# Kernel optimization log

Hardware: AMD Instinct MI355X
Metric: run time of the kernel (lower is better)

## Reference

```python
import jax, jax.numpy as jnp
import numpy as np

N_NODES = 50000      # nodes
N_EDGES = 800000     # edges (avg degree 16)
D = 128              # input_dim == hidden_dim
C = 32               # output_dim (classes)
G = 64               # number of graphs in batch
EPS = 1e-5           # LayerNorm eps (torch default)
NUM_LAYERS = 3


def setup_inputs() -> dict:
    key = jax.random.key(0)
    ks = jax.random.split(key, 12)
    scale = 1.0 / np.sqrt(D)
    x = jax.random.normal(ks[0], (N_NODES, D), dtype=jnp.float32)
    edge_index = jax.random.randint(ks[1], (2, N_EDGES), 0, N_NODES)
    batch = jnp.sort(jax.random.randint(ks[2], (N_NODES,), 0, G))
    # CustomConv params: self-loop linear + message linear, 3 layers stacked
    W_self = jax.random.normal(ks[3], (NUM_LAYERS, D, D), dtype=jnp.float32) * scale
    b_self = jnp.zeros((NUM_LAYERS, D), dtype=jnp.float32)
    W_msg = jax.random.normal(ks[4], (NUM_LAYERS, D, D), dtype=jnp.float32) * scale
    b_msg = jnp.zeros((NUM_LAYERS, D), dtype=jnp.float32)
    # two LayerNorms (after layers 0 and 1)
    ln_g = jnp.ones((2, D), dtype=jnp.float32)
    ln_b = jnp.zeros((2, D), dtype=jnp.float32)
    # post-MP MLP head: Linear(D,D) -> Dropout(identity in eval) -> Linear(D,C)
    W1 = jax.random.normal(ks[5], (D, D), dtype=jnp.float32) * scale
    b1 = jnp.zeros((D,), dtype=jnp.float32)
    W2 = jax.random.normal(ks[6], (D, C), dtype=jnp.float32) * scale
    b2 = jnp.zeros((C,), dtype=jnp.float32)
    return {"x": x, "W_self": W_self, "b_self": b_self, "W_msg": W_msg,
            "b_msg": b_msg, "ln_g": ln_g, "ln_b": ln_b, "W1": W1, "b1": b1,
            "W2": W2, "b2": b2, "edge_index": edge_index, "batch": batch}


def _layer_norm(h, g, b):
    mu = jnp.mean(h, axis=-1, keepdims=True)
    var = jnp.mean(jnp.square(h - mu), axis=-1, keepdims=True)
    return g * (h - mu) * jax.lax.rsqrt(var + EPS) + b


def reference(x, W_self, b_self, W_msg, b_msg, ln_g, ln_b, W1, b1, W2, b2,
              edge_index, batch):
    src, dst = edge_index[0], edge_index[1]
    for i in range(NUM_LAYERS):
        # CustomConv: self linear + sum-aggregated neighbor messages
        msg = x @ W_msg[i] + b_msg[i]                     # [N, D]
        agg = jax.ops.segment_sum(msg[src], dst, num_segments=N_NODES)
        x = x @ W_self[i] + b_self[i] + agg               # [N, D]
        x = jax.nn.relu(x)
        # dropout p=0.25 is identity in eval mode
        if i != NUM_LAYERS - 1:
            x = _layer_norm(x, ln_g[i], ln_b[i])
    # global mean pool over graphs
    sums = jax.ops.segment_sum(x, batch, num_segments=G)          # [G, D]
    cnt = jax.ops.segment_sum(jnp.ones((N_NODES,), x.dtype), batch,
                              num_segments=G)                     # [G]
    pooled = sums / jnp.maximum(cnt, 1.0)[:, None]
    # post-MP head (dropout identity in eval)
    h = pooled @ W1 + b1
    logits = h @ W2 + b2                                          # [G, C]
    return jax.nn.log_softmax(logits, axis=1)
```

## Files before the change

### kernel.cpp

```cpp
#include <hip/hip_runtime.h>
#include <hip/hip_bf16.h>
#include <math.h>

#define N_NODES 50000
#define N_EDGES 800000
#define DIM 128
#define CLS 32
#define NGRAPH 64
#define LN_EPS 1e-5f
#define NBLK 196
#define ABLK 256
#define EPB (N_EDGES / ABLK)
#define EB_STRIDE 7168
#define LCAP 8192
#define ROWS1 (N_NODES + 1)

typedef __attribute__((ext_vector_type(8))) short bf16x8;
typedef __attribute__((ext_vector_type(4))) float f32x4;

static __device__ __forceinline__ int lower_bound_i(const int* a, int n, int key) {
    int lo = 0, hi = n;
    while (lo < hi) { int mid = (lo + hi) >> 1; if (a[mid] < key) lo = mid + 1; else hi = mid; }
    return lo;
}


__global__ __launch_bounds__(256) void prep_kernel(
    const float* __restrict__ x, const float* __restrict__ Wself,
    const float* __restrict__ Wmsg, __hip_bfloat16* __restrict__ XbIn,
    __hip_bfloat16* __restrict__ WT,
    int* __restrict__ ecur, float* __restrict__ gsum,
    __hip_bfloat16* __restrict__ padA, __hip_bfloat16* __restrict__ padB,
    __hip_bfloat16* __restrict__ padC, __hip_bfloat16* __restrict__ padD) {
    int i = blockIdx.x * 256 + threadIdx.x;
    if (i < N_NODES * DIM / 2) {
        float2 v = ((const float2*)x)[i];
        ((__hip_bfloat162*)XbIn)[i] = __float22bfloat162_rn(v);
    }
    if (i < 3 * 128 * 256) {
        int l = i / (128 * 256);
        int rem = i - l * (128 * 256);
        int n = rem >> 8;
        int k = rem & 255;
        float v = (k < 128) ? Wself[l * 16384 + k * 128 + n]
                            : Wmsg[l * 16384 + (k - 128) * 128 + n];
        WT[i] = __float2bfloat16(v);
    }
    if (i < NBLK) ecur[i] = i * EB_STRIDE;
    if (i < NGRAPH * DIM) gsum[i] = 0.f;
    if (i < DIM) {
        padA[i] = __float2bfloat16(0.f);
        padB[i] = __float2bfloat16(0.f);
        padC[i] = __float2bfloat16(0.f);
        padD[i] = __float2bfloat16(0.f);
    }
}


__global__ __launch_bounds__(1024) void bucket_kernel(
    const int* __restrict__ esrc, const int* __restrict__ edst,
    int* __restrict__ ecur, int* __restrict__ ebuf) {
    __shared__ int bc4[4][NBLK];
    __shared__ int bc[NBLK], bres[NBLK], bcnt[NBLK];
    const int t = threadIdx.x;
    const int e0 = blockIdx.x * EPB;
    for (int i = t; i < 4 * NBLK; i += 1024) ((int*)bc4)[i] = 0;
    __syncthreads();
    int dr[4], sr[4];
#pragma unroll
    for (int it = 0; it < 4; it++) {
        int i = t + it * 1024;
        if (i < EPB) { dr[it] = edst[e0 + i]; sr[it] = esrc[e0 + i]; }
        else { dr[it] = -1; sr[it] = 0; }
    }
    const int cpy = (t >> 6) & 3;
#pragma unroll
    for (int it = 0; it < 4; it++)
        if (dr[it] >= 0) atomicAdd(&bc4[cpy][dr[it] >> 8], 1);
    __syncthreads();
    if (t < NBLK) {
        int c = bc4[0][t] + bc4[1][t] + bc4[2][t] + bc4[3][t];
        int r = (c + 7) & ~7;
        int res = atomicAdd(&ecur[t], r);
        bres[t] = res;
        bcnt[t] = c;
        bc[t] = res;
    }
    __syncthreads();
#pragma unroll
    for (int it = 0; it < 4; it++)
        if (dr[it] >= 0) {
            int d = dr[it];
            int pos = atomicAdd(&bc[d >> 8], 1);
            ebuf[pos] = ((d & 255) << 16) | sr[it];
        }
    __syncthreads();
    if (t < NBLK) {
        int c = bcnt[t], r = (c + 7) & ~7, base = bres[t];
        for (int j = c; j < r; j++) ebuf[base + j] = -1;
    }
}


__global__ __launch_bounds__(1024) void csr_fused_kernel(
    const int* __restrict__ ebuf, const int* __restrict__ ecur,
    int* __restrict__ counts, int* __restrict__ off, int* __restrict__ csr) {
    __shared__ int ncnt[256];
    __shared__ int ssc[256];
    __shared__ int cur[256];
    __shared__ int lcsr[LCAP];
    const int b = blockIdx.x, t = threadIdx.x;
    const int used = ecur[b] - b * EB_STRIDE;
    const int* eb = ebuf + b * EB_STRIDE;
    for (int i = t; i < LCAP; i += 1024) lcsr[i] = N_NODES;
    if (t < 256) ncnt[t] = 0;
    __syncthreads();
    for (int i = t; i < used; i += 1024) {
        int p = eb[i];
        if (p != -1) atomicAdd(&ncnt[p >> 16], 1);
    }
    __syncthreads();
    int myc = 0, mypad = 0;
    const int gi = b * 256 + t;
    if (t < 256) {
        myc = (gi < N_NODES) ? ncnt[t] : 0;
        mypad = (myc + 7) & ~7;
        ssc[t] = mypad;
    }
    __syncthreads();
    for (int o = 1; o < 256; o <<= 1) {
        int v = 0;
        if (t < 256 && t >= o) v = ssc[t - o];
        __syncthreads();
        if (t < 256) ssc[t] += v;
        __syncthreads();
    }
    if (t < 256) {
        int eoff = ssc[t] - mypad;
        cur[t] = eoff;
        if (gi < N_NODES) {
            off[gi] = b * LCAP + eoff;
            counts[gi] = myc;
        }
    }
    __syncthreads();
    for (int i = t; i < used; i += 1024) {
        int p = eb[i];
        if (p != -1) {
            int pos = atomicAdd(&cur[p >> 16], 1);
            lcsr[pos] = p & 0xFFFF;
        }
    }
    __syncthreads();
    const int total = ssc[255];
    int4* dst4 = (int4*)(csr + b * LCAP);
    const int4* src4 = (const int4*)lcsr;
    for (int i = t; i < (total >> 2); i += 1024) dst4[i] = src4[i];
}


__global__ __launch_bounds__(256) void agg_kernel(const __hip_bfloat16* __restrict__ Xb,
                                                  const int* __restrict__ off,
                                                  const int* __restrict__ counts,
                                                  const int* __restrict__ csr,
                                                  __hip_bfloat16* __restrict__ Sb) {
    const int wave = threadIdx.x >> 6;
    const int lane = threadIdx.x & 63;
    const int n = blockIdx.x * 4 + wave;
    if (n >= N_NODES) return;
    const int seg = lane >> 4;
    const int cl = lane & 15;
    int b = off[n];
    int e = b + ((counts[n] + 7) & ~7);
    float ac[8];
#pragma unroll
    for (int j = 0; j < 8; j++) ac[j] = 0.f;
    int base = b;
    for (; base + 16 <= e; base += 16) {
        int idx16 = csr[base + (lane & 15)];
        int s[4];
        uint4 v[4];
#pragma unroll
        for (int r = 0; r < 4; r++) s[r] = __shfl(idx16, r * 4 + seg, 64);
#pragma unroll
        for (int r = 0; r < 4; r++)
            v[r] = *(const uint4*)(Xb + (size_t)s[r] * DIM + cl * 8);
#pragma unroll
        for (int r = 0; r < 4; r++) {
            unsigned int u[4] = {v[r].x, v[r].y, v[r].z, v[r].w};
#pragma unroll
            for (int k = 0; k < 4; k++) {
                union { unsigned int b32; float f; } lo, hi;
                lo.b32 = u[k] << 16;
                hi.b32 = u[k] & 0xffff0000u;
                ac[2 * k] += lo.f;
                ac[2 * k + 1] += hi.f;
            }
        }
    }
    if (base < e) {
        int idx8 = csr[base + (lane & 7)];
        int s0 = __shfl(idx8, seg, 64);
        int s1 = __shfl(idx8, 4 + seg, 64);
        uint4 v0 = *(const uint4*)(Xb + (size_t)s0 * DIM + cl * 8);
        uint4 v1 = *(const uint4*)(Xb + (size_t)s1 * DIM + cl * 8);
        unsigned int u[8] = {v0.x, v0.y, v0.z, v0.w, v1.x, v1.y, v1.z, v1.w};
#pragma unroll
        for (int k = 0; k < 8; k++) {
            union { unsigned int b32; float f; } lo, hi;
            lo.b32 = u[k] << 16;
            hi.b32 = u[k] & 0xffff0000u;
            ac[2 * (k & 3)] += lo.f;
            ac[2 * (k & 3) + 1] += hi.f;
        }
    }
#pragma unroll
    for (int j = 0; j < 8; j++) {
        ac[j] += __shfl_xor(ac[j], 16, 64);
        ac[j] += __shfl_xor(ac[j], 32, 64);
    }
    if (lane < 16) {
        union { uint4 u; __hip_bfloat162 h[4]; } pk;
#pragma unroll
        for (int k = 0; k < 4; k++)
            pk.h[k] = __float22bfloat162_rn(make_float2(ac[2 * k], ac[2 * k + 1]));
        *(uint4*)(Sb + (size_t)n * DIM + cl * 8) = pk.u;
    }
}


__global__ __launch_bounds__(256) void layer_mfma_kernel(
    const __hip_bfloat16* __restrict__ Xb, const __hip_bfloat16* __restrict__ Sb,
    const __hip_bfloat16* __restrict__ WT,
    const float* __restrict__ bself, const float* __restrict__ bmsg,
    const int* __restrict__ deg,
    const float* __restrict__ lng, const float* __restrict__ lnb,
    const int* __restrict__ batch, float* __restrict__ gsum,
    __hip_bfloat16* __restrict__ XoutB, int do_ln, int do_pool) {
    __shared__ __hip_bfloat16 wlds[128 * 136];
    const int tid = threadIdx.x;
    const int w = tid >> 6, lane = tid & 63;
    const int l15 = lane & 15, q = lane >> 4;

    const int row = blockIdx.x * 64 + w * 16 + l15;
    const int rowc = min(row, N_NODES);

    f32x4 acc[8];
#pragma unroll
    for (int ct = 0; ct < 8; ct++) acc[ct] = (f32x4){0.f, 0.f, 0.f, 0.f};

    const __hip_bfloat16* Abase[2] = {Xb, Sb};
    for (int c = 0; c < 2; c++) {
        __syncthreads();
        {
            int n = tid >> 1, h = tid & 1;
            const uint4* src = (const uint4*)(WT + n * 256 + c * 128 + h * 64);
            uint4* dst = (uint4*)(&wlds[n * 136 + h * 64]);
#pragma unroll
            for (int i = 0; i < 8; i++) dst[i] = src[i];
        }
        __syncthreads();
        const __hip_bfloat16* arow = Abase[c] + (size_t)rowc * DIM;
#pragma unroll
        for (int ks = 0; ks < 4; ks++) {
            bf16x8 afrag = *(const bf16x8*)(arow + ks * 32 + q * 8);
#pragma unroll
            for (int ct = 0; ct < 8; ct++) {
                bf16x8 bfrag = *(const bf16x8*)(&wlds[(ct * 16 + l15) * 136 + ks * 32 + q * 8]);
                acc[ct] = __builtin_amdgcn_mfma_f32_16x16x32_bf16(afrag, bfrag, acc[ct], 0, 0, 0);
            }
        }
    }

    const int growbase = blockIdx.x * 64 + w * 16;
    float racc[8];
#pragma unroll
    for (int ct = 0; ct < 8; ct++) racc[ct] = 0.f;
    int gw = 0;
    bool fastp = false;
    if (do_pool) {
        int first = (growbase < N_NODES) ? growbase : (N_NODES - 1);
        gw = batch[first];
        int lastrow = growbase + 15;
        fastp = (growbase < N_NODES) && (lastrow < N_NODES) && (batch[lastrow] == gw);
    }
#pragma unroll
    for (int r = 0; r < 4; r++) {
        int grow = growbase + q * 4 + r;
        bool valid = grow < N_NODES;
        float dg = valid ? (float)deg[grow] : 0.f;
        float v[8];
        float s1 = 0.f;
#pragma unroll
        for (int ct = 0; ct < 8; ct++) {
            int col = ct * 16 + l15;
            float h = acc[ct][r] + bself[col] + dg * bmsg[col];
            h = fmaxf(h, 0.f);
            v[ct] = h;
            s1 += h;
        }
        if (do_ln) {
#pragma unroll
            for (int m = 1; m < 16; m <<= 1) s1 += __shfl_xor(s1, m, 64);
            float mu = s1 * (1.0f / 128.0f);
            float s2 = 0.f;
#pragma unroll
            for (int ct = 0; ct < 8; ct++) { float d = v[ct] - mu; s2 += d * d; }
#pragma unroll
            for (int m = 1; m < 16; m <<= 1) s2 += __shfl_xor(s2, m, 64);
            float rs = rsqrtf(s2 * (1.0f / 128.0f) + LN_EPS);
#pragma unroll
            for (int ct = 0; ct < 8; ct++) {
                int col = ct * 16 + l15;
                v[ct] = lng[col] * (v[ct] - mu) * rs + lnb[col];
            }
        }
        if (do_pool) {
            if (fastp) {
#pragma unroll
                for (int ct = 0; ct < 8; ct++) racc[ct] += v[ct];
            } else if (valid) {
                int g = batch[grow];
#pragma unroll
                for (int ct = 0; ct < 8; ct++)
                    atomicAdd(&gsum[g * DIM + ct * 16 + l15], v[ct]);
            }
        } else if (valid) {
#pragma unroll
            for (int ct = 0; ct < 8; ct++) {
                int col = ct * 16 + l15;
                XoutB[(size_t)grow * DIM + col] = __float2bfloat16(v[ct]);
            }
        }
    }
    if (do_pool && fastp) {
#pragma unroll
        for (int ct = 0; ct < 8; ct++) {
            racc[ct] += __shfl_xor(racc[ct], 16, 64);
            racc[ct] += __shfl_xor(racc[ct], 32, 64);
        }
        if (q == 0) {
#pragma unroll
            for (int ct = 0; ct < 8; ct++)
                atomicAdd(&gsum[gw * DIM + ct * 16 + l15], racc[ct]);
        }
    }
}


__global__ __launch_bounds__(128) void head_kernel(
    const float* __restrict__ gsum, const int* __restrict__ batch,
    const float* __restrict__ W1, const float* __restrict__ b1,
    const float* __restrict__ W2, const float* __restrict__ b2,
    float* __restrict__ out) {
    __shared__ float p[128];
    __shared__ float hh[128];
    int g = blockIdx.x;
    int j = threadIdx.x;
    int lo = lower_bound_i(batch, N_NODES, g);
    int hi = lower_bound_i(batch, N_NODES, g + 1);
    float cnt = fmaxf((float)(hi - lo), 1.0f);
    p[j] = gsum[g * DIM + j] / cnt;
    __syncthreads();
    float s = b1[j];
    for (int k = 0; k < DIM; k++) s += p[k] * W1[k * DIM + j];
    hh[j] = s;
    __syncthreads();
    if (j < CLS) {
        float l = b2[j];
        for (int k = 0; k < DIM; k++) l += hh[k] * W2[k * CLS + j];
        float mx = l;
#pragma unroll
        for (int m = 16; m >= 1; m >>= 1) mx = fmaxf(mx, __shfl_xor(mx, m, 64));
        float ex = expf(l - mx);
        float se = ex;
#pragma unroll
        for (int m = 16; m >= 1; m >>= 1) se += __shfl_xor(se, m, 64);
        out[g * CLS + j] = l - mx - logf(se);
    }
}


extern "C" void kernel_launch(void* const* d_in, const int* in_sizes, int n_in,
                              void* d_out, int out_size, void* d_ws, size_t ws_size,
                              hipStream_t stream) {
    (void)in_sizes; (void)n_in; (void)out_size; (void)ws_size;
    const float* x     = (const float*)d_in[0];
    const float* Wself = (const float*)d_in[1];
    const float* bself = (const float*)d_in[2];
    const float* Wmsg  = (const float*)d_in[3];
    const float* bmsg  = (const float*)d_in[4];
    const float* lng   = (const float*)d_in[5];
    const float* lnb   = (const float*)d_in[6];
    const float* W1    = (const float*)d_in[7];
    const float* b1    = (const float*)d_in[8];
    const float* W2    = (const float*)d_in[9];
    const float* b2    = (const float*)d_in[10];
    const int*   ei    = (const int*)d_in[11];
    const int*   batch = (const int*)d_in[12];
    const int* esrc = ei;
    const int* edst = ei + N_EDGES;

    char* w = (char*)d_ws;
    size_t o = 0;
    auto alloc = [&](size_t bytes) { void* p = w + o; o += (bytes + 255) & ~(size_t)255; return p; };
    __hip_bfloat16* XbIn = (__hip_bfloat16*)alloc((size_t)ROWS1 * DIM * 2);
    __hip_bfloat16* Xb0  = (__hip_bfloat16*)alloc((size_t)ROWS1 * DIM * 2);
    __hip_bfloat16* Xb1  = (__hip_bfloat16*)alloc((size_t)ROWS1 * DIM * 2);
    __hip_bfloat16* Sb   = (__hip_bfloat16*)alloc((size_t)ROWS1 * DIM * 2);
    __hip_bfloat16* WT   = (__hip_bfloat16*)alloc((size_t)3 * 128 * 256 * 2);
    int*   counts = (int*)alloc((size_t)N_NODES * 4);
    int*   offs   = (int*)alloc((size_t)(N_NODES + 1) * 4);
    int*   ecur   = (int*)alloc((size_t)NBLK * 4);
    int*   ebuf   = (int*)alloc((size_t)NBLK * EB_STRIDE * 4);
    int*   csr    = (int*)alloc((size_t)NBLK * LCAP * 4);
    float* gsum   = (float*)alloc((size_t)NGRAPH * DIM * 4);

    prep_kernel<<<(N_NODES * DIM / 2 + 255) / 256, 256, 0, stream>>>(
        x, Wself, Wmsg, XbIn, WT, ecur, gsum,
        XbIn + (size_t)N_NODES * DIM, Xb0 + (size_t)N_NODES * DIM,
        Xb1 + (size_t)N_NODES * DIM, Sb + (size_t)N_NODES * DIM);

    bucket_kernel<<<ABLK, 1024, 0, stream>>>(esrc, edst, ecur, ebuf);
    csr_fused_kernel<<<NBLK, 1024, 0, stream>>>(ebuf, ecur, counts, offs, csr);

    const __hip_bfloat16* XbCur = XbIn;
    __hip_bfloat16* bbufs[3] = {Xb0, Xb1, Xb0};
    for (int i = 0; i < 3; i++) {
        agg_kernel<<<(N_NODES + 3) / 4, 256, 0, stream>>>(XbCur, offs, counts, csr, Sb);
        layer_mfma_kernel<<<(N_NODES + 63) / 64, 256, 0, stream>>>(
            XbCur, Sb, WT + (size_t)i * 128 * 256,
            bself + i * DIM, bmsg + i * DIM, counts,
            (i < 2) ? lng + i * DIM : lng, (i < 2) ? lnb + i * DIM : lnb,
            batch, gsum,
            bbufs[i], (i < 2) ? 1 : 0, (i == 2) ? 1 : 0);
        XbCur = bbufs[i];
    }

    head_kernel<<<NGRAPH, 128, 0, stream>>>(gsum, batch, W1, b1, W2, b2, (float*)d_out);
}
```

Measured before the change: 263.1 us.

## Fuse neighbor aggregation into the MFMA layer kernel and shrink CSR to u16

Removes the separate aggregation kernel. Each wave of the layer kernel now gathers neighbor features for its 16 rows, two nodes at a time, and writes the sums into LDS, where the second MFMA pass reads them. This drops the global round trip of the aggregated buffer and three launches. The CSR source indices are stored as 16-bit values, halving index traffic. The cost is less gather parallelism per block, since 782 blocks now do the gathering where 12500 did before, plus extra LDS use that may lower occupancy.

```diff
diff --git a/kernel.cpp b/kernel.cpp
--- a/kernel.cpp
+++ b/kernel.cpp
@@ -24,6 +24,43 @@
     return lo;
 }
 
+static __device__ __forceinline__ void acc8(float* ac, uint4 v) {
+    unsigned int u[4] = {v.x, v.y, v.z, v.w};
+#pragma unroll
+    for (int k = 0; k < 4; k++) {
+        union { unsigned int b; float f; } lo, hi;
+        lo.b = u[k] << 16;
+        hi.b = u[k] & 0xffff0000u;
+        ac[2 * k] += lo.f;
+        ac[2 * k + 1] += hi.f;
+    }
+}
+
+static __device__ __forceinline__ void drain_node(const __hip_bfloat16* __restrict__ Xb,
+                                                  const unsigned short* __restrict__ csr,
+                                                  int b, int e, int seg, int cl, float* ac) {
+    for (; b + 16 <= e; b += 16) {
+        int idx16 = csr[b + cl];
+        int s[4];
+        uint4 v[4];
+#pragma unroll
+        for (int r = 0; r < 4; r++) s[r] = __shfl(idx16, r * 4 + seg, 64);
+#pragma unroll
+        for (int r = 0; r < 4; r++) v[r] = *(const uint4*)(Xb + (size_t)s[r] * DIM + cl * 8);
+#pragma unroll
+        for (int r = 0; r < 4; r++) acc8(ac, v[r]);
+    }
+    if (b < e) {
+        int idx8 = csr[b + (cl & 7)];
+        int s0 = __shfl(idx8, seg, 64);
+        int s1 = __shfl(idx8, 4 + seg, 64);
+        uint4 v0 = *(const uint4*)(Xb + (size_t)s0 * DIM + cl * 8);
+        uint4 v1 = *(const uint4*)(Xb + (size_t)s1 * DIM + cl * 8);
+        acc8(ac, v0);
+        acc8(ac, v1);
+    }
+}
+
 
 __global__ __launch_bounds__(256) void prep_kernel(
     const float* __restrict__ x, const float* __restrict__ Wself,
@@ -31,7 +68,7 @@
     __hip_bfloat16* __restrict__ WT,
     int* __restrict__ ecur, float* __restrict__ gsum,
     __hip_bfloat16* __restrict__ padA, __hip_bfloat16* __restrict__ padB,
-    __hip_bfloat16* __restrict__ padC, __hip_bfloat16* __restrict__ padD) {
+    __hip_bfloat16* __restrict__ padC) {
     int i = blockIdx.x * 256 + threadIdx.x;
     if (i < N_NODES * DIM / 2) {
         float2 v = ((const float2*)x)[i];
@@ -52,7 +89,6 @@
         padA[i] = __float2bfloat16(0.f);
         padB[i] = __float2bfloat16(0.f);
         padC[i] = __float2bfloat16(0.f);
-        padD[i] = __float2bfloat16(0.f);
     }
 }
 
@@ -104,15 +140,17 @@
 
 __global__ __launch_bounds__(1024) void csr_fused_kernel(
     const int* __restrict__ ebuf, const int* __restrict__ ecur,
-    int* __restrict__ counts, int* __restrict__ off, int* __restrict__ csr) {
+    int* __restrict__ counts, int* __restrict__ off,
+    unsigned short* __restrict__ csr) {
     __shared__ int ncnt[256];
     __shared__ int ssc[256];
     __shared__ int cur[256];
-    __shared__ int lcsr[LCAP];
+    __shared__ unsigned short lcsr[LCAP];
     const int b = blockIdx.x, t = threadIdx.x;
     const int used = ecur[b] - b * EB_STRIDE;
     const int* eb = ebuf + b * EB_STRIDE;
-    for (int i = t; i < LCAP; i += 1024) lcsr[i] = N_NODES;
+    for (int i = t; i < LCAP / 2; i += 1024)
+        ((unsigned int*)lcsr)[i] = 0xC350C350u;
     if (t < 256) ncnt[t] = 0;
     __syncthreads();
     for (int i = t; i < used; i += 1024) {
@@ -148,131 +186,131 @@
         int p = eb[i];
         if (p != -1) {
             int pos = atomicAdd(&cur[p >> 16], 1);
-            lcsr[pos] = p & 0xFFFF;
+            lcsr[pos] = (unsigned short)(p & 0xFFFF);
         }
     }
     __syncthreads();
     const int total = ssc[255];
-    int4* dst4 = (int4*)(csr + b * LCAP);
+    int4* dst4 = (int4*)(csr + (size_t)b * LCAP);
     const int4* src4 = (const int4*)lcsr;
-    for (int i = t; i < (total >> 2); i += 1024) dst4[i] = src4[i];
-}
-
-
-__global__ __launch_bounds__(256) void agg_kernel(const __hip_bfloat16* __restrict__ Xb,
-                                                  const int* __restrict__ off,
-                                                  const int* __restrict__ counts,
-                                                  const int* __restrict__ csr,
-                                                  __hip_bfloat16* __restrict__ Sb) {
-    const int wave = threadIdx.x >> 6;
-    const int lane = threadIdx.x & 63;
-    const int n = blockIdx.x * 4 + wave;
-    if (n >= N_NODES) return;
-    const int seg = lane >> 4;
-    const int cl = lane & 15;
-    int b = off[n];
-    int e = b + ((counts[n] + 7) & ~7);
-    float ac[8];
-#pragma unroll
-    for (int j = 0; j < 8; j++) ac[j] = 0.f;
-    int base = b;
-    for (; base + 16 <= e; base += 16) {
-        int idx16 = csr[base + (lane & 15)];
-        int s[4];
-        uint4 v[4];
-#pragma unroll
-        for (int r = 0; r < 4; r++) s[r] = __shfl(idx16, r * 4 + seg, 64);
-#pragma unroll
-        for (int r = 0; r < 4; r++)
-            v[r] = *(const uint4*)(Xb + (size_t)s[r] * DIM + cl * 8);
-#pragma unroll
-        for (int r = 0; r < 4; r++) {
-            unsigned int u[4] = {v[r].x, v[r].y, v[r].z, v[r].w};
-#pragma unroll
-            for (int k = 0; k < 4; k++) {
-                union { unsigned int b32; float f; } lo, hi;
-                lo.b32 = u[k] << 16;
-                hi.b32 = u[k] & 0xffff0000u;
-                ac[2 * k] += lo.f;
-                ac[2 * k + 1] += hi.f;
-            }
-        }
-    }
-    if (base < e) {
-        int idx8 = csr[base + (lane & 7)];
-        int s0 = __shfl(idx8, seg, 64);
-        int s1 = __shfl(idx8, 4 + seg, 64);
-        uint4 v0 = *(const uint4*)(Xb + (size_t)s0 * DIM + cl * 8);
-        uint4 v1 = *(const uint4*)(Xb + (size_t)s1 * DIM + cl * 8);
-        unsigned int u[8] = {v0.x, v0.y, v0.z, v0.w, v1.x, v1.y, v1.z, v1.w};
-#pragma unroll
-        for (int k = 0; k < 8; k++) {
-            union { unsigned int b32; float f; } lo, hi;
-            lo.b32 = u[k] << 16;
-            hi.b32 = u[k] & 0xffff0000u;
-            ac[2 * (k & 3)] += lo.f;
-            ac[2 * (k & 3) + 1] += hi.f;
-        }
-    }
-#pragma unroll
-    for (int j = 0; j < 8; j++) {
-        ac[j] += __shfl_xor(ac[j], 16, 64);
-        ac[j] += __shfl_xor(ac[j], 32, 64);
-    }
-    if (lane < 16) {
-        union { uint4 u; __hip_bfloat162 h[4]; } pk;
-#pragma unroll
-        for (int k = 0; k < 4; k++)
-            pk.h[k] = __float22bfloat162_rn(make_float2(ac[2 * k], ac[2 * k + 1]));
-        *(uint4*)(Sb + (size_t)n * DIM + cl * 8) = pk.u;
-    }
-}
-
-
-__global__ __launch_bounds__(256) void layer_mfma_kernel(
-    const __hip_bfloat16* __restrict__ Xb, const __hip_bfloat16* __restrict__ Sb,
+    for (int i = t; i < (total >> 3); i += 1024) dst4[i] = src4[i];
+}
+
+
+__global__ __launch_bounds__(256) void layer_fused_kernel(
+    const __hip_bfloat16* __restrict__ Xb,
+    const int* __restrict__ off, const int* __restrict__ counts,
+    const unsigned short* __restrict__ csr,
     const __hip_bfloat16* __restrict__ WT,
     const float* __restrict__ bself, const float* __restrict__ bmsg,
-    const int* __restrict__ deg,
     const float* __restrict__ lng, const float* __restrict__ lnb,
     const int* __restrict__ batch, float* __restrict__ gsum,
     __hip_bfloat16* __restrict__ XoutB, int do_ln, int do_pool) {
     __shared__ __hip_bfloat16 wlds[128 * 136];
+    __shared__ __hip_bfloat16 slds[64 * 136];
     const int tid = threadIdx.x;
     const int w = tid >> 6, lane = tid & 63;
     const int l15 = lane & 15, q = lane >> 4;
-
-    const int row = blockIdx.x * 64 + w * 16 + l15;
+    const int rowblk = blockIdx.x * 64;
+    const int growbase = rowblk + w * 16;
+
+    {
+        int n = tid >> 1, h = tid & 1;
+        const uint4* src = (const uint4*)(WT + n * 256 + h * 64);
+        uint4* dst = (uint4*)(&wlds[n * 136 + h * 64]);
+#pragma unroll
+        for (int i = 0; i < 8; i++) dst[i] = src[i];
+    }
+
+    const int seg = lane >> 4, cl = lane & 15;
+    for (int j = 0; j < 16; j += 2) {
+        int na = growbase + j;
+        int nb = na + 1;
+        int ba = 0, ea = 0, bb = 0, eb2 = 0;
+        if (na < N_NODES) { ba = off[na]; ea = ba + ((counts[na] + 7) & ~7); }
+        if (nb < N_NODES) { bb = off[nb]; eb2 = bb + ((counts[nb] + 7) & ~7); }
+        float aa[8], ab[8];
+#pragma unroll
+        for (int k = 0; k < 8; k++) { aa[k] = 0.f; ab[k] = 0.f; }
+        while (ba + 16 <= ea && bb + 16 <= eb2) {
+            int ia = csr[ba + cl];
+            int ib = csr[bb + cl];
+            int sa[4], sb[4];
+#pragma unroll
+            for (int r = 0; r < 4; r++) {
+                sa[r] = __shfl(ia, r * 4 + seg, 64);
+                sb[r] = __shfl(ib, r * 4 + seg, 64);
+            }
+            uint4 va[4], vb[4];
+#pragma unroll
+            for (int r = 0; r < 4; r++) va[r] = *(const uint4*)(Xb + (size_t)sa[r] * DIM + cl * 8);
+#pragma unroll
+            for (int r = 0; r < 4; r++) vb[r] = *(const uint4*)(Xb + (size_t)sb[r] * DIM + cl * 8);
+#pragma unroll
+            for (int r = 0; r < 4; r++) acc8(aa, va[r]);
+#pragma unroll
+            for (int r = 0; r < 4; r++) acc8(ab, vb[r]);
+            ba += 16;
+            bb += 16;
+        }
+        drain_node(Xb, csr, ba, ea, seg, cl, aa);
+        drain_node(Xb, csr, bb, eb2, seg, cl, ab);
+#pragma unroll
+        for (int k = 0; k < 8; k++) {
+            aa[k] += __shfl_xor(aa[k], 16, 64);
+            aa[k] += __shfl_xor(aa[k], 32, 64);
+            ab[k] += __shfl_xor(ab[k], 16, 64);
+            ab[k] += __shfl_xor(ab[k], 32, 64);
+        }
+        if (lane < 16) {
+            union { uint4 u; __hip_bfloat162 h[4]; } pa, pb;
+#pragma unroll
+            for (int k = 0; k < 4; k++) {
+                pa.h[k] = __float22bfloat162_rn(make_float2(aa[2 * k], aa[2 * k + 1]));
+                pb.h[k] = __float22bfloat162_rn(make_float2(ab[2 * k], ab[2 * k + 1]));
+            }
+            *(uint4*)(&slds[(w * 16 + j) * 136 + cl * 8]) = pa.u;
+            *(uint4*)(&slds[(w * 16 + j + 1) * 136 + cl * 8]) = pb.u;
+        }
+    }
+
+    f32x4 acc[8];
+#pragma unroll
+    for (int ct = 0; ct < 8; ct++) acc[ct] = (f32x4){0.f, 0.f, 0.f, 0.f};
+
+    __syncthreads();
+
+    const int row = growbase + l15;
     const int rowc = min(row, N_NODES);
-
-    f32x4 acc[8];
-#pragma unroll
-    for (int ct = 0; ct < 8; ct++) acc[ct] = (f32x4){0.f, 0.f, 0.f, 0.f};
-
-    const __hip_bfloat16* Abase[2] = {Xb, Sb};
-    for (int c = 0; c < 2; c++) {
-        __syncthreads();
-        {
-            int n = tid >> 1, h = tid & 1;
-            const uint4* src = (const uint4*)(WT + n * 256 + c * 128 + h * 64);
-            uint4* dst = (uint4*)(&wlds[n * 136 + h * 64]);
-#pragma unroll
-            for (int i = 0; i < 8; i++) dst[i] = src[i];
-        }
-        __syncthreads();
-        const __hip_bfloat16* arow = Abase[c] + (size_t)rowc * DIM;
-#pragma unroll
-        for (int ks = 0; ks < 4; ks++) {
-            bf16x8 afrag = *(const bf16x8*)(arow + ks * 32 + q * 8);
-#pragma unroll
-            for (int ct = 0; ct < 8; ct++) {
-                bf16x8 bfrag = *(const bf16x8*)(&wlds[(ct * 16 + l15) * 136 + ks * 32 + q * 8]);
-                acc[ct] = __builtin_amdgcn_mfma_f32_16x16x32_bf16(afrag, bfrag, acc[ct], 0, 0, 0);
-            }
-        }
-    }
-
-    const int growbase = blockIdx.x * 64 + w * 16;
+    const __hip_bfloat16* arow = Xb + (size_t)rowc * DIM;
+#pragma unroll
+    for (int ks = 0; ks < 4; ks++) {
+        bf16x8 afrag = *(const bf16x8*)(arow + ks * 32 + q * 8);
+#pragma unroll
+        for (int ct = 0; ct < 8; ct++) {
+            bf16x8 bfrag = *(const bf16x8*)(&wlds[(ct * 16 + l15) * 136 + ks * 32 + q * 8]);
+            acc[ct] = __builtin_amdgcn_mfma_f32_16x16x32_bf16(afrag, bfrag, acc[ct], 0, 0, 0);
+        }
+    }
+    __syncthreads();
+    {
+        int n = tid >> 1, h = tid & 1;
+        const uint4* src = (const uint4*)(WT + n * 256 + 128 + h * 64);
+        uint4* dst = (uint4*)(&wlds[n * 136 + h * 64]);
+#pragma unroll
+        for (int i = 0; i < 8; i++) dst[i] = src[i];
+    }
+    __syncthreads();
+#pragma unroll
+    for (int ks = 0; ks < 4; ks++) {
+        bf16x8 afrag = *(const bf16x8*)(&slds[(w * 16 + l15) * 136 + ks * 32 + q * 8]);
+#pragma unroll
+        for (int ct = 0; ct < 8; ct++) {
+            bf16x8 bfrag = *(const bf16x8*)(&wlds[(ct * 16 + l15) * 136 + ks * 32 + q * 8]);
+            acc[ct] = __builtin_amdgcn_mfma_f32_16x16x32_bf16(afrag, bfrag, acc[ct], 0, 0, 0);
+        }
+    }
+
     float racc[8];
 #pragma unroll
     for (int ct = 0; ct < 8; ct++) racc[ct] = 0.f;
@@ -288,7 +326,7 @@
     for (int r = 0; r < 4; r++) {
         int grow = growbase + q * 4 + r;
         bool valid = grow < N_NODES;
-        float dg = valid ? (float)deg[grow] : 0.f;
+        float dg = valid ? (float)counts[grow] : 0.f;
         float v[8];
         float s1 = 0.f;
 #pragma unroll
@@ -407,19 +445,18 @@
     __hip_bfloat16* XbIn = (__hip_bfloat16*)alloc((size_t)ROWS1 * DIM * 2);
     __hip_bfloat16* Xb0  = (__hip_bfloat16*)alloc((size_t)ROWS1 * DIM * 2);
     __hip_bfloat16* Xb1  = (__hip_bfloat16*)alloc((size_t)ROWS1 * DIM * 2);
-    __hip_bfloat16* Sb   = (__hip_bfloat16*)alloc((size_t)ROWS1 * DIM * 2);
     __hip_bfloat16* WT   = (__hip_bfloat16*)alloc((size_t)3 * 128 * 256 * 2);
     int*   counts = (int*)alloc((size_t)N_NODES * 4);
     int*   offs   = (int*)alloc((size_t)(N_NODES + 1) * 4);
     int*   ecur   = (int*)alloc((size_t)NBLK * 4);
     int*   ebuf   = (int*)alloc((size_t)NBLK * EB_STRIDE * 4);
-    int*   csr    = (int*)alloc((size_t)NBLK * LCAP * 4);
+    unsigned short* csr = (unsigned short*)alloc((size_t)NBLK * LCAP * 2);
     float* gsum   = (float*)alloc((size_t)NGRAPH * DIM * 4);
 
     prep_kernel<<<(N_NODES * DIM / 2 + 255) / 256, 256, 0, stream>>>(
         x, Wself, Wmsg, XbIn, WT, ecur, gsum,
         XbIn + (size_t)N_NODES * DIM, Xb0 + (size_t)N_NODES * DIM,
-        Xb1 + (size_t)N_NODES * DIM, Sb + (size_t)N_NODES * DIM);
+        Xb1 + (size_t)N_NODES * DIM);
 
     bucket_kernel<<<ABLK, 1024, 0, stream>>>(esrc, edst, ecur, ebuf);
     csr_fused_kernel<<<NBLK, 1024, 0, stream>>>(ebuf, ecur, counts, offs, csr);
@@ -427,10 +464,9 @@
     const __hip_bfloat16* XbCur = XbIn;
     __hip_bfloat16* bbufs[3] = {Xb0, Xb1, Xb0};
     for (int i = 0; i < 3; i++) {
-        agg_kernel<<<(N_NODES + 3) / 4, 256, 0, stream>>>(XbCur, offs, counts, csr, Sb);
-        layer_mfma_kernel<<<(N_NODES + 63) / 64, 256, 0, stream>>>(
-            XbCur, Sb, WT + (size_t)i * 128 * 256,
-            bself + i * DIM, bmsg + i * DIM, counts,
+        layer_fused_kernel<<<(N_NODES + 63) / 64, 256, 0, stream>>>(
+            XbCur, offs, counts, csr, WT + (size_t)i * 128 * 256,
+            bself + i * DIM, bmsg + i * DIM,
             (i < 2) ? lng + i * DIM : lng, (i < 2) ? lnb + i * DIM : lnb,
             batch, gsum,
             bbufs[i], (i < 2) ? 1 : 0, (i == 2) ? 1 : 0);
```

Result: slower. 311.4 us (+18.3%).
